# Optimization experiments

Measured on AMD Instinct MI355X. Metric: run time of the kernel, lower is better.

Reference implementation:

```python
import jax, jax.numpy as jnp
import numpy as np

DELTA_VAR = 0.5
DELTA_DIST = 1.5
ALPHA = 1.0
BETA = 1.0
GAMMA = 0.001
NUM_INST = 32  # instance ids are 1..NUM_INST; 0 = background


def setup_inputs() -> dict:
    key = jax.random.key(0)
    k1, k2 = jax.random.split(key)
    embeddings = jax.random.normal(k1, (4, 16, 512, 512), dtype=jnp.float32)
    instance_labels = jax.random.randint(k2, (4, 512, 512), 0, NUM_INST + 1, dtype=jnp.int32)
    return {"embeddings": embeddings, "instance_labels": instance_labels}


def reference(embeddings, instance_labels):
    B, E, H, W = embeddings.shape
    HW = H * W
    S = NUM_INST + 1  # segment slots per batch incl. background slot 0

    emb = embeddings.transpose(0, 2, 3, 1).reshape(B, HW, E)   # [B, HW, E]
    lab = instance_labels.reshape(B, HW)                        # [B, HW]

    # ---- per-(batch, instance) means via one segment reduction ----
    seg = (jnp.arange(B, dtype=lab.dtype)[:, None] * S + lab).reshape(-1)
    sums = jax.ops.segment_sum(emb.reshape(-1, E), seg, num_segments=B * S).reshape(B, S, E)
    counts = jax.ops.segment_sum(jnp.ones((B * HW,), emb.dtype), seg, num_segments=B * S).reshape(B, S)
    means = sums / jnp.maximum(counts, 1.0)[..., None]          # [B, S, E]

    present = counts[:, 1:] > 0                                  # [B, K] instances only
    n = present.sum(-1).astype(emb.dtype)                        # [B] num_instances
    n_safe = jnp.maximum(n, 1.0)

    # ---- variance (pull) term: hinge(||e - mean||_2 - delta_var) ----
    mean_per_pix = jnp.take_along_axis(means, lab[:, :, None], axis=1)  # [B, HW, E]
    diff = emb - mean_per_pix
    pix_dist = jnp.sqrt(jnp.sum(diff * diff, axis=-1))           # [B, HW] (norm=2)
    hinge = jnp.maximum(pix_dist - DELTA_VAR, 0.0) * (lab > 0).astype(emb.dtype)
    var_loss = hinge.sum(-1) / n_safe                            # [B]

    # ---- distance (push) term: pairwise hinge(2*delta_dist - ||mi - mj||) ----
    m = means[:, 1:]                                             # [B, K, E]
    d2 = jnp.sum((m[:, :, None, :] - m[:, None, :, :]) ** 2, -1)  # [B, K, K]
    upper = jnp.triu(jnp.ones((NUM_INST, NUM_INST), bool), 1)
    pair_mask = upper[None] & present[:, :, None] & present[:, None, :]
    d = jnp.sqrt(jnp.where(pair_mask, d2, 1.0))
    pair_hinge = jnp.where(pair_mask, jnp.maximum(2.0 * DELTA_DIST - d, 0.0), 0.0)
    num_pairs = n * (n - 1.0) / 2.0
    dist_loss = jnp.where(n > 1, pair_hinge.sum((-1, -2)) / jnp.maximum(num_pairs, 1.0), 0.0)  # [B]

    # ---- regularization term: ||mean||_2 averaged over instances ----
    mnorm = jnp.sqrt(jnp.where(present, jnp.sum(m * m, -1), 1.0))
    reg_loss = jnp.where(present, mnorm, 0.0).sum(-1) / n_safe   # [B]

    total = ALPHA * var_loss.mean() + BETA * dist_loss.mean() + GAMMA * reg_loss.mean()
    return total
```

## Files before the change

### kernel.cpp

```cpp
#include <hip/hip_runtime.h>

#define NB 4
#define NE 16
#define NHW (512*512)
#define NINST 32
#define SP 17
#define DELTA_VAR 0.5f
#define DELTA_DIST 1.5f
#define ALPHA 1.0f
#define BETA 1.0f
#define GAMMA 0.001f

typedef __attribute__((ext_vector_type(8))) short short8;
typedef __attribute__((ext_vector_type(4))) float f32x4;

#define T_SUM 0
#define T_CNT (NB*NINST*NE)
#define T_MEAN (T_CNT + NB*NINST)
#define T_VARP (T_MEAN + NB*33*NE)
#define T_DIST (T_VARP+NB)
#define T_REG  (T_DIST+NB)
#define T_NS   (T_REG+NB)
#define T_TOTAL (T_NS+NB)

#define GRID_H 1024
#define BLK_H 256
#define BPB_H (GRID_H/NB)
#define PXB 1024
#define PXW 256
#define ITERS_H 4
#define GRID_V 1024
#define BLK_V 256
#define BPB_V (GRID_V/NB)

__device__ __forceinline__ unsigned f2bf(float x) {
    unsigned u = __builtin_bit_cast(unsigned, x);
    return (u + 0x7FFFu + ((u >> 16) & 1u)) >> 16;
}

__device__ __forceinline__ float wave_sum(float v) {
    #pragma unroll
    for (int o = 32; o > 0; o >>= 1) v += __shfl_down(v, o, 64);
    return v;
}

union PK { unsigned u[4]; short8 s; };

__global__ __launch_bounds__(BLK_H) void k_hist(const float* __restrict__ emb,
        const int* __restrict__ lab, float* __restrict__ tbl) {
    __shared__ float red[4][2*NE][SP];
    __shared__ float redc[4][2*NE];
    const int t = threadIdx.x;
    const int lane = t & 63;
    const int wv = t >> 6;
    const int colg = lane >> 4;
    const int cm = lane & 15;
    const int b = blockIdx.x / BPB_H;
    const int blk = blockIdx.x % BPB_H;

    const float* ebase = emb + (size_t)b*(NE*NHW) + (size_t)cm*NHW;
    const int* lbase = lab + (size_t)b*NHW;

    f32x4 acc_s0 = {0.f,0.f,0.f,0.f}, acc_s1 = {0.f,0.f,0.f,0.f};
    f32x4 acc_c0 = {0.f,0.f,0.f,0.f}, acc_c1 = {0.f,0.f,0.f,0.f};
    PK ones; ones.u[0]=ones.u[1]=ones.u[2]=ones.u[3]=0x3F803F80u;

    const int base = blk*PXB + wv*PXW;
    for (int it = 0; it < ITERS_H; ++it) {
        #pragma unroll
        for (int u2 = 0; u2 < 2; ++u2) {
            const int ko = base + it*64 + u2*32 + colg*8;
            const float4 v0 = *(const float4*)(ebase + ko);
            const float4 v1 = *(const float4*)(ebase + ko + 4);
            const int4 L0 = *(const int4*)(lbase + ko);
            const int4 L1 = *(const int4*)(lbase + ko + 4);
            PK bf;
            bf.u[0] = f2bf(v0.x) | (f2bf(v0.y) << 16);
            bf.u[1] = f2bf(v0.z) | (f2bf(v0.w) << 16);
            bf.u[2] = f2bf(v1.x) | (f2bf(v1.y) << 16);
            bf.u[3] = f2bf(v1.z) | (f2bf(v1.w) << 16);
            const int la[8] = {L0.x,L0.y,L0.z,L0.w,L1.x,L1.y,L1.z,L1.w};
            PK a0, a1;
            #pragma unroll
            for (int p = 0; p < 4; ++p) {
                const unsigned lo0 = (la[2*p]   == cm+1 ) ? 0x3F80u : 0u;
                const unsigned hi0 = (la[2*p+1] == cm+1 ) ? 0x3F80u : 0u;
                const unsigned lo1 = (la[2*p]   == cm+17) ? 0x3F80u : 0u;
                const unsigned hi1 = (la[2*p+1] == cm+17) ? 0x3F80u : 0u;
                a0.u[p] = lo0 | (hi0 << 16);
                a1.u[p] = lo1 | (hi1 << 16);
            }
            acc_s0 = __builtin_amdgcn_mfma_f32_16x16x32_bf16(a0.s, bf.s,  acc_s0, 0,0,0);
            acc_s1 = __builtin_amdgcn_mfma_f32_16x16x32_bf16(a1.s, bf.s,  acc_s1, 0,0,0);
            acc_c0 = __builtin_amdgcn_mfma_f32_16x16x32_bf16(a0.s, ones.s, acc_c0, 0,0,0);
            acc_c1 = __builtin_amdgcn_mfma_f32_16x16x32_bf16(a1.s, ones.s, acc_c1, 0,0,0);
        }
    }
    #pragma unroll
    for (int r = 0; r < 4; ++r) {
        red[wv][colg*4 + r][cm]      = acc_s0[r];
        red[wv][16 + colg*4 + r][cm] = acc_s1[r];
    }
    if (cm == 0) {
        #pragma unroll
        for (int r = 0; r < 4; ++r) {
            redc[wv][colg*4 + r]      = acc_c0[r];
            redc[wv][16 + colg*4 + r] = acc_c1[r];
        }
    }
    __syncthreads();
    for (int i = t; i < NINST*NE; i += BLK_H) {
        const int s = i >> 4, e = i & 15;
        const float v = red[0][s][e] + red[1][s][e] + red[2][s][e] + red[3][s][e];
        atomicAdd(&tbl[T_SUM + b*NINST*NE + i], v);
    }
    if (t < NINST) {
        const float v = redc[0][t] + redc[1][t] + redc[2][t] + redc[3][t];
        atomicAdd(&tbl[T_CNT + b*NINST + t], v);
    }
}

__global__ void k_stats(float* __restrict__ tbl) {
    const int b = blockIdx.x;
    const int lane = threadIdx.x;
    __shared__ float lcnt[NINST];
    __shared__ float lmean[NINST*SP];
    __shared__ int lpres[NINST];
    if (lane < NINST) {
        const float c = tbl[T_CNT + b*NINST + lane];
        lcnt[lane] = c;
        lpres[lane] = (c > 0.f) ? 1 : 0;
    }
    __syncthreads();
    for (int i = lane; i < NINST*NE; i += 64) {
        const int s = i >> 4, e = i & 15;
        const float m = tbl[T_SUM + b*NINST*NE + i] / fmaxf(lcnt[s], 1.f);
        lmean[s*SP + e] = m;
        tbl[T_MEAN + b*33*NE + (s+1)*NE + e] = m;
    }
    if (lane < NE) tbl[T_MEAN + b*33*NE + lane] = 0.f;
    __syncthreads();
    const int n = __popcll(__ballot((lane < NINST) ? (lpres[lane] != 0) : false));
    float dsum = 0.f;
    for (int idx = lane; idx < NINST*NINST; idx += 64) {
        const int i = idx >> 5, j = idx & 31;
        if (i < j && lpres[i] && lpres[j]) {
            float d2 = 0.f;
            #pragma unroll
            for (int e = 0; e < NE; e++) {
                const float df = lmean[i*SP+e] - lmean[j*SP+e];
                d2 += df*df;
            }
            dsum += fmaxf(2.f*DELTA_DIST - sqrtf(d2), 0.f);
        }
    }
    dsum = wave_sum(dsum);
    float rsum = 0.f;
    if (lane < NINST && lpres[lane]) {
        float s2 = 0.f;
        #pragma unroll
        for (int e = 0; e < NE; e++) { const float m = lmean[lane*SP+e]; s2 += m*m; }
        rsum = sqrtf(s2);
    }
    rsum = wave_sum(rsum);
    if (lane == 0) {
        const float nf = (float)n;
        const float nsafe = fmaxf(nf, 1.f);
        tbl[T_DIST+b] = (n > 1) ? dsum / fmaxf(nf*(nf-1.f)*0.5f, 1.f) : 0.f;
        tbl[T_REG+b] = rsum / nsafe;
        tbl[T_NS+b] = nsafe;
    }
}

__global__ __launch_bounds__(BLK_V) void k_var(const float* __restrict__ emb,
        const int* __restrict__ lab, float* __restrict__ tbl) {
    __shared__ float lmean[33*SP];
    __shared__ float lvar;
    const int t = threadIdx.x;
    const int b = blockIdx.x / BPB_V;
    const int blk = blockIdx.x % BPB_V;
    for (int i = t; i < 33*NE; i += BLK_V) {
        const int s = i >> 4, e = i & 15;
        lmean[s*SP+e] = tbl[T_MEAN + b*33*NE + i];
        (void)s; (void)e;
    }
    __syncthreads();
    if (t == 0) lvar = 0.f;
    __syncthreads();
    const float* ebase = emb + (size_t)b*(NE*NHW);
    const int* lbase = lab + (size_t)b*NHW;
    float acc = 0.f;
    for (int q = blk*BLK_V + t; q < NHW/4; q += BPB_V*BLK_V) {
        const int p = q*4;
        const int4 l4 = *(const int4*)(lbase + p);
        const int o0 = l4.x*SP, o1 = l4.y*SP, o2 = l4.z*SP, o3 = l4.w*SP;
        float d0=0.f, d1=0.f, d2=0.f, d3=0.f;
        #pragma unroll
        for (int e = 0; e < NE; e++) {
            const float4 v = *(const float4*)(ebase + (size_t)e*NHW + p);
            float df;
            df = v.x - lmean[o0+e]; d0 += df*df;
            df = v.y - lmean[o1+e]; d1 += df*df;
            df = v.z - lmean[o2+e]; d2 += df*df;
            df = v.w - lmean[o3+e]; d3 += df*df;
        }
        if (l4.x > 0) acc += fmaxf(sqrtf(d0) - DELTA_VAR, 0.f);
        if (l4.y > 0) acc += fmaxf(sqrtf(d1) - DELTA_VAR, 0.f);
        if (l4.z > 0) acc += fmaxf(sqrtf(d2) - DELTA_VAR, 0.f);
        if (l4.w > 0) acc += fmaxf(sqrtf(d3) - DELTA_VAR, 0.f);
    }
    const float w = wave_sum(acc);
    if ((t & 63) == 0) atomicAdd(&lvar, w);
    __syncthreads();
    if (t == 0) atomicAdd(&tbl[T_VARP+b], lvar);
}

__global__ void k_final(const float* __restrict__ tbl, float* __restrict__ out) {
    if (threadIdx.x == 0 && blockIdx.x == 0) {
        float tot = 0.f;
        for (int b = 0; b < NB; b++) {
            tot += ALPHA * (tbl[T_VARP+b] / tbl[T_NS+b])
                 + BETA * tbl[T_DIST+b]
                 + GAMMA * tbl[T_REG+b];
        }
        out[0] = tot * (1.f/NB);
    }
}

extern "C" void kernel_launch(void* const* d_in, const int* in_sizes, int n_in,
                              void* d_out, int out_size, void* d_ws, size_t ws_size,
                              hipStream_t stream) {
    const float* emb = (const float*)d_in[0];
    const int* lab = (const int*)d_in[1];
    float* out = (float*)d_out;
    float* tbl = (float*)d_ws;

    hipMemsetAsync(d_ws, 0, (size_t)T_TOTAL*sizeof(float), stream);
    k_hist<<<GRID_H, BLK_H, 0, stream>>>(emb, lab, tbl);
    k_stats<<<NB, 64, 0, stream>>>(tbl);
    k_var<<<GRID_V, BLK_V, 0, stream>>>(emb, lab, tbl);
    k_final<<<1, 64, 0, stream>>>(tbl, out);
}
```

Baseline: 61.90 us.

## Replace global atomics with per-block partials and replicate means in LDS

The histogram kernel now writes per-block partial sums to workspace with 256 blocks of 512 threads, and the stats kernel reduces them. This removes the global atomics and the memset launch. The variance kernel drops its grid-stride loop so each thread handles one group of four pixels. It also loads means from a 4-way replicated, 20-float-padded LDS table as float4 vectors to cut bank conflicts. Per-block variance partials are summed in the final kernel instead of through atomics. The cost is more workspace traffic and a serial partial reduction over 64 blocks in k_stats.

```diff
diff --git a/kernel.cpp b/kernel.cpp
--- a/kernel.cpp
+++ b/kernel.cpp
@@ -4,7 +4,6 @@
 #define NE 16
 #define NHW (512*512)
 #define NINST 32
-#define SP 17
 #define DELTA_VAR 0.5f
 #define DELTA_DIST 1.5f
 #define ALPHA 1.0f
@@ -14,25 +13,28 @@
 typedef __attribute__((ext_vector_type(8))) short short8;
 typedef __attribute__((ext_vector_type(4))) float f32x4;
 
-#define T_SUM 0
-#define T_CNT (NB*NINST*NE)
-#define T_MEAN (T_CNT + NB*NINST)
-#define T_VARP (T_MEAN + NB*33*NE)
-#define T_DIST (T_VARP+NB)
-#define T_REG  (T_DIST+NB)
-#define T_NS   (T_REG+NB)
-#define T_TOTAL (T_NS+NB)
-
-#define GRID_H 1024
-#define BLK_H 256
+#define PH_STRIDE 544
+#define GRID_H 256
+#define P_HIST 0
+#define T_MEAN (GRID_H*PH_STRIDE)
+#define T_MEAN_SZ (33*16)
+#define T_DIST (T_MEAN + NB*T_MEAN_SZ)
+#define T_REG  (T_DIST + NB)
+#define T_NS   (T_REG + NB)
+#define V_PART (T_NS + NB)
+
+#define BLK_H 512
 #define BPB_H (GRID_H/NB)
-#define PXB 1024
-#define PXW 256
-#define ITERS_H 4
+#define PXB_H 4096
+#define PXW_H 512
+#define CHUNKS_H 16
 #define GRID_V 1024
 #define BLK_V 256
 #define BPB_V (GRID_V/NB)
 
+#define LMREP 4
+#define LMSTR 668
+
 __device__ __forceinline__ unsigned f2bf(float x) {
     unsigned u = __builtin_bit_cast(unsigned, x);
     return (u + 0x7FFFu + ((u >> 16) & 1u)) >> 16;
@@ -47,9 +49,9 @@
 union PK { unsigned u[4]; short8 s; };
 
 __global__ __launch_bounds__(BLK_H) void k_hist(const float* __restrict__ emb,
-        const int* __restrict__ lab, float* __restrict__ tbl) {
-    __shared__ float red[4][2*NE][SP];
-    __shared__ float redc[4][2*NE];
+        const int* __restrict__ lab, float* __restrict__ ws) {
+    __shared__ float red[8][2*NE][17];
+    __shared__ float redc[8][2*NE];
     const int t = threadIdx.x;
     const int lane = t & 63;
     const int wv = t >> 6;
@@ -65,36 +67,34 @@
     f32x4 acc_c0 = {0.f,0.f,0.f,0.f}, acc_c1 = {0.f,0.f,0.f,0.f};
     PK ones; ones.u[0]=ones.u[1]=ones.u[2]=ones.u[3]=0x3F803F80u;
 
-    const int base = blk*PXB + wv*PXW;
-    for (int it = 0; it < ITERS_H; ++it) {
+    const int base = blk*PXB_H + wv*PXW_H;
+    #pragma unroll 4
+    for (int it = 0; it < CHUNKS_H; ++it) {
+        const int ko = base + it*32 + colg*8;
+        const float4 v0 = *(const float4*)(ebase + ko);
+        const float4 v1 = *(const float4*)(ebase + ko + 4);
+        const int4 L0 = *(const int4*)(lbase + ko);
+        const int4 L1 = *(const int4*)(lbase + ko + 4);
+        PK bf;
+        bf.u[0] = f2bf(v0.x) | (f2bf(v0.y) << 16);
+        bf.u[1] = f2bf(v0.z) | (f2bf(v0.w) << 16);
+        bf.u[2] = f2bf(v1.x) | (f2bf(v1.y) << 16);
+        bf.u[3] = f2bf(v1.z) | (f2bf(v1.w) << 16);
+        const int la[8] = {L0.x,L0.y,L0.z,L0.w,L1.x,L1.y,L1.z,L1.w};
+        PK a0, a1;
         #pragma unroll
-        for (int u2 = 0; u2 < 2; ++u2) {
-            const int ko = base + it*64 + u2*32 + colg*8;
-            const float4 v0 = *(const float4*)(ebase + ko);
-            const float4 v1 = *(const float4*)(ebase + ko + 4);
-            const int4 L0 = *(const int4*)(lbase + ko);
-            const int4 L1 = *(const int4*)(lbase + ko + 4);
-            PK bf;
-            bf.u[0] = f2bf(v0.x) | (f2bf(v0.y) << 16);
-            bf.u[1] = f2bf(v0.z) | (f2bf(v0.w) << 16);
-            bf.u[2] = f2bf(v1.x) | (f2bf(v1.y) << 16);
-            bf.u[3] = f2bf(v1.z) | (f2bf(v1.w) << 16);
-            const int la[8] = {L0.x,L0.y,L0.z,L0.w,L1.x,L1.y,L1.z,L1.w};
-            PK a0, a1;
-            #pragma unroll
-            for (int p = 0; p < 4; ++p) {
-                const unsigned lo0 = (la[2*p]   == cm+1 ) ? 0x3F80u : 0u;
-                const unsigned hi0 = (la[2*p+1] == cm+1 ) ? 0x3F80u : 0u;
-                const unsigned lo1 = (la[2*p]   == cm+17) ? 0x3F80u : 0u;
-                const unsigned hi1 = (la[2*p+1] == cm+17) ? 0x3F80u : 0u;
-                a0.u[p] = lo0 | (hi0 << 16);
-                a1.u[p] = lo1 | (hi1 << 16);
-            }
-            acc_s0 = __builtin_amdgcn_mfma_f32_16x16x32_bf16(a0.s, bf.s,  acc_s0, 0,0,0);
-            acc_s1 = __builtin_amdgcn_mfma_f32_16x16x32_bf16(a1.s, bf.s,  acc_s1, 0,0,0);
-            acc_c0 = __builtin_amdgcn_mfma_f32_16x16x32_bf16(a0.s, ones.s, acc_c0, 0,0,0);
-            acc_c1 = __builtin_amdgcn_mfma_f32_16x16x32_bf16(a1.s, ones.s, acc_c1, 0,0,0);
-        }
+        for (int p = 0; p < 4; ++p) {
+            const unsigned lo0 = (la[2*p]   == cm+1 ) ? 0x3F80u : 0u;
+            const unsigned hi0 = (la[2*p+1] == cm+1 ) ? 0x3F80u : 0u;
+            const unsigned lo1 = (la[2*p]   == cm+17) ? 0x3F80u : 0u;
+            const unsigned hi1 = (la[2*p+1] == cm+17) ? 0x3F80u : 0u;
+            a0.u[p] = lo0 | (hi0 << 16);
+            a1.u[p] = lo1 | (hi1 << 16);
+        }
+        acc_s0 = __builtin_amdgcn_mfma_f32_16x16x32_bf16(a0.s, bf.s,   acc_s0, 0,0,0);
+        acc_s1 = __builtin_amdgcn_mfma_f32_16x16x32_bf16(a1.s, bf.s,   acc_s1, 0,0,0);
+        acc_c0 = __builtin_amdgcn_mfma_f32_16x16x32_bf16(a0.s, ones.s, acc_c0, 0,0,0);
+        acc_c1 = __builtin_amdgcn_mfma_f32_16x16x32_bf16(a1.s, ones.s, acc_c1, 0,0,0);
     }
     #pragma unroll
     for (int r = 0; r < 4; ++r) {
@@ -109,119 +109,153 @@
         }
     }
     __syncthreads();
-    for (int i = t; i < NINST*NE; i += BLK_H) {
+    float* dst = ws + P_HIST + (size_t)blockIdx.x*PH_STRIDE;
+    for (int i = t; i < PH_STRIDE; i += BLK_H) {
+        float v;
+        if (i < 512) {
+            const int s = i >> 4, e = i & 15;
+            v = red[0][s][e]+red[1][s][e]+red[2][s][e]+red[3][s][e]
+              + red[4][s][e]+red[5][s][e]+red[6][s][e]+red[7][s][e];
+        } else {
+            const int s = i - 512;
+            v = redc[0][s]+redc[1][s]+redc[2][s]+redc[3][s]
+              + redc[4][s]+redc[5][s]+redc[6][s]+redc[7][s];
+        }
+        dst[i] = v;
+    }
+}
+
+__global__ void k_stats(float* __restrict__ ws) {
+    const int b = blockIdx.x;
+    const int t = threadIdx.x;
+    __shared__ float lred[PH_STRIDE];
+    __shared__ float lmean[NINST*17];
+    __shared__ float lcnt[NINST];
+    __shared__ int lpres[NINST];
+    const float* ph = ws + P_HIST + (size_t)(b*BPB_H)*PH_STRIDE;
+    for (int i = t; i < PH_STRIDE; i += 256) {
+        float s = 0.f;
+        #pragma unroll 8
+        for (int k = 0; k < BPB_H; k++) s += ph[(size_t)k*PH_STRIDE + i];
+        lred[i] = s;
+    }
+    __syncthreads();
+    if (t < NINST) {
+        const float c = lred[512 + t];
+        lcnt[t] = c;
+        lpres[t] = (c > 0.f) ? 1 : 0;
+    }
+    __syncthreads();
+    for (int i = t; i < 512; i += 256) {
         const int s = i >> 4, e = i & 15;
-        const float v = red[0][s][e] + red[1][s][e] + red[2][s][e] + red[3][s][e];
-        atomicAdd(&tbl[T_SUM + b*NINST*NE + i], v);
-    }
-    if (t < NINST) {
-        const float v = redc[0][t] + redc[1][t] + redc[2][t] + redc[3][t];
-        atomicAdd(&tbl[T_CNT + b*NINST + t], v);
-    }
-}
-
-__global__ void k_stats(float* __restrict__ tbl) {
-    const int b = blockIdx.x;
-    const int lane = threadIdx.x;
-    __shared__ float lcnt[NINST];
-    __shared__ float lmean[NINST*SP];
-    __shared__ int lpres[NINST];
-    if (lane < NINST) {
-        const float c = tbl[T_CNT + b*NINST + lane];
-        lcnt[lane] = c;
-        lpres[lane] = (c > 0.f) ? 1 : 0;
-    }
-    __syncthreads();
-    for (int i = lane; i < NINST*NE; i += 64) {
-        const int s = i >> 4, e = i & 15;
-        const float m = tbl[T_SUM + b*NINST*NE + i] / fmaxf(lcnt[s], 1.f);
-        lmean[s*SP + e] = m;
-        tbl[T_MEAN + b*33*NE + (s+1)*NE + e] = m;
-    }
-    if (lane < NE) tbl[T_MEAN + b*33*NE + lane] = 0.f;
-    __syncthreads();
-    const int n = __popcll(__ballot((lane < NINST) ? (lpres[lane] != 0) : false));
-    float dsum = 0.f;
-    for (int idx = lane; idx < NINST*NINST; idx += 64) {
-        const int i = idx >> 5, j = idx & 31;
-        if (i < j && lpres[i] && lpres[j]) {
-            float d2 = 0.f;
+        lmean[s*17 + e] = lred[i] / fmaxf(lcnt[s], 1.f);
+    }
+    __syncthreads();
+    for (int i = t; i < 33*NE; i += 256) {
+        const int l = i >> 4, e = i & 15;
+        ws[T_MEAN + b*T_MEAN_SZ + i] = (l == 0) ? 0.f : lmean[(l-1)*17 + e];
+    }
+    if (t < 64) {
+        const int lane = t;
+        const int n = __popcll(__ballot((lane < NINST) ? (lpres[lane] != 0) : false));
+        float dsum = 0.f;
+        for (int idx = lane; idx < NINST*NINST; idx += 64) {
+            const int i = idx >> 5, j = idx & 31;
+            if (i < j && lpres[i] && lpres[j]) {
+                float d2 = 0.f;
+                #pragma unroll
+                for (int e = 0; e < NE; e++) {
+                    const float df = lmean[i*17+e] - lmean[j*17+e];
+                    d2 += df*df;
+                }
+                dsum += fmaxf(2.f*DELTA_DIST - sqrtf(d2), 0.f);
+            }
+        }
+        dsum = wave_sum(dsum);
+        float rsum = 0.f;
+        if (lane < NINST && lpres[lane]) {
+            float s2 = 0.f;
             #pragma unroll
-            for (int e = 0; e < NE; e++) {
-                const float df = lmean[i*SP+e] - lmean[j*SP+e];
-                d2 += df*df;
-            }
-            dsum += fmaxf(2.f*DELTA_DIST - sqrtf(d2), 0.f);
-        }
-    }
-    dsum = wave_sum(dsum);
-    float rsum = 0.f;
-    if (lane < NINST && lpres[lane]) {
-        float s2 = 0.f;
-        #pragma unroll
-        for (int e = 0; e < NE; e++) { const float m = lmean[lane*SP+e]; s2 += m*m; }
-        rsum = sqrtf(s2);
-    }
-    rsum = wave_sum(rsum);
-    if (lane == 0) {
-        const float nf = (float)n;
-        const float nsafe = fmaxf(nf, 1.f);
-        tbl[T_DIST+b] = (n > 1) ? dsum / fmaxf(nf*(nf-1.f)*0.5f, 1.f) : 0.f;
-        tbl[T_REG+b] = rsum / nsafe;
-        tbl[T_NS+b] = nsafe;
+            for (int e = 0; e < NE; e++) { const float m = lmean[lane*17+e]; s2 += m*m; }
+            rsum = sqrtf(s2);
+        }
+        rsum = wave_sum(rsum);
+        if (lane == 0) {
+            const float nf = (float)n;
+            const float nsafe = fmaxf(nf, 1.f);
+            ws[T_DIST+b] = (n > 1) ? dsum / fmaxf(nf*(nf-1.f)*0.5f, 1.f) : 0.f;
+            ws[T_REG+b] = rsum / nsafe;
+            ws[T_NS+b] = nsafe;
+        }
     }
 }
 
 __global__ __launch_bounds__(BLK_V) void k_var(const float* __restrict__ emb,
-        const int* __restrict__ lab, float* __restrict__ tbl) {
-    __shared__ float lmean[33*SP];
-    __shared__ float lvar;
-    const int t = threadIdx.x;
-    const int b = blockIdx.x / BPB_V;
-    const int blk = blockIdx.x % BPB_V;
-    for (int i = t; i < 33*NE; i += BLK_V) {
-        const int s = i >> 4, e = i & 15;
-        lmean[s*SP+e] = tbl[T_MEAN + b*33*NE + i];
-        (void)s; (void)e;
-    }
-    __syncthreads();
-    if (t == 0) lvar = 0.f;
-    __syncthreads();
+        const int* __restrict__ lab, float* __restrict__ ws) {
+    __shared__ __align__(16) float lm[LMREP*LMSTR];
+    __shared__ float wred[4];
+    const int t = threadIdx.x;
+    const int b = blockIdx.x >> 8;
+    const int blk = blockIdx.x & 255;
+    for (int c4 = 0; c4 < LMREP; ++c4) {
+        for (int i = t; i < 33*20; i += BLK_V) {
+            const int l = i / 20, e = i % 20;
+            if (e < 16) lm[c4*LMSTR + i] = ws[T_MEAN + b*T_MEAN_SZ + l*16 + e];
+        }
+    }
+    __syncthreads();
+    const float* lmc = lm + ((t >> 4) & (LMREP-1))*LMSTR;
     const float* ebase = emb + (size_t)b*(NE*NHW);
     const int* lbase = lab + (size_t)b*NHW;
+
+    const int p = (blk*BLK_V + t)*4;
+    const int4 l4 = *(const int4*)(lbase + p);
+    float4 m0[4], m1[4], m2[4], m3[4];
+    {
+        const float4* q0 = (const float4*)(lmc + l4.x*20);
+        const float4* q1 = (const float4*)(lmc + l4.y*20);
+        const float4* q2 = (const float4*)(lmc + l4.z*20);
+        const float4* q3 = (const float4*)(lmc + l4.w*20);
+        #pragma unroll
+        for (int c = 0; c < 4; ++c) { m0[c]=q0[c]; m1[c]=q1[c]; m2[c]=q2[c]; m3[c]=q3[c]; }
+    }
+    float d0=0.f, d1=0.f, d2=0.f, d3=0.f;
+    #pragma unroll
+    for (int e = 0; e < NE; e++) {
+        const float4 v = *(const float4*)(ebase + (size_t)e*NHW + p);
+        float df;
+        df = v.x - ((const float*)&m0[e>>2])[e&3]; d0 += df*df;
+        df = v.y - ((const float*)&m1[e>>2])[e&3]; d1 += df*df;
+        df = v.z - ((const float*)&m2[e>>2])[e&3]; d2 += df*df;
+        df = v.w - ((const float*)&m3[e>>2])[e&3]; d3 += df*df;
+    }
     float acc = 0.f;
-    for (int q = blk*BLK_V + t; q < NHW/4; q += BPB_V*BLK_V) {
-        const int p = q*4;
-        const int4 l4 = *(const int4*)(lbase + p);
-        const int o0 = l4.x*SP, o1 = l4.y*SP, o2 = l4.z*SP, o3 = l4.w*SP;
-        float d0=0.f, d1=0.f, d2=0.f, d3=0.f;
-        #pragma unroll
-        for (int e = 0; e < NE; e++) {
-            const float4 v = *(const float4*)(ebase + (size_t)e*NHW + p);
-            float df;
-            df = v.x - lmean[o0+e]; d0 += df*df;
-            df = v.y - lmean[o1+e]; d1 += df*df;
-            df = v.z - lmean[o2+e]; d2 += df*df;
-            df = v.w - lmean[o3+e]; d3 += df*df;
-        }
-        if (l4.x > 0) acc += fmaxf(sqrtf(d0) - DELTA_VAR, 0.f);
-        if (l4.y > 0) acc += fmaxf(sqrtf(d1) - DELTA_VAR, 0.f);
-        if (l4.z > 0) acc += fmaxf(sqrtf(d2) - DELTA_VAR, 0.f);
-        if (l4.w > 0) acc += fmaxf(sqrtf(d3) - DELTA_VAR, 0.f);
-    }
-    const float w = wave_sum(acc);
-    if ((t & 63) == 0) atomicAdd(&lvar, w);
-    __syncthreads();
-    if (t == 0) atomicAdd(&tbl[T_VARP+b], lvar);
-}
-
-__global__ void k_final(const float* __restrict__ tbl, float* __restrict__ out) {
-    if (threadIdx.x == 0 && blockIdx.x == 0) {
+    if (l4.x > 0) acc += fmaxf(sqrtf(d0) - DELTA_VAR, 0.f);
+    if (l4.y > 0) acc += fmaxf(sqrtf(d1) - DELTA_VAR, 0.f);
+    if (l4.z > 0) acc += fmaxf(sqrtf(d2) - DELTA_VAR, 0.f);
+    if (l4.w > 0) acc += fmaxf(sqrtf(d3) - DELTA_VAR, 0.f);
+
+    const float wsum = wave_sum(acc);
+    if ((t & 63) == 0) wred[t >> 6] = wsum;
+    __syncthreads();
+    if (t == 0) ws[V_PART + blockIdx.x] = wred[0]+wred[1]+wred[2]+wred[3];
+}
+
+__global__ void k_final(const float* __restrict__ ws, float* __restrict__ out) {
+    const int t = threadIdx.x;
+    __shared__ float vb[4];
+    float s = 0.f;
+    #pragma unroll
+    for (int k = 0; k < 4; ++k) s += ws[V_PART + t*4 + k];
+    s = wave_sum(s);
+    if ((t & 63) == 0) vb[t >> 6] = s;
+    __syncthreads();
+    if (t == 0) {
         float tot = 0.f;
         for (int b = 0; b < NB; b++) {
-            tot += ALPHA * (tbl[T_VARP+b] / tbl[T_NS+b])
-                 + BETA * tbl[T_DIST+b]
-                 + GAMMA * tbl[T_REG+b];
+            tot += ALPHA * (vb[b] / ws[T_NS+b])
+                 + BETA * ws[T_DIST+b]
+                 + GAMMA * ws[T_REG+b];
         }
         out[0] = tot * (1.f/NB);
     }
@@ -233,11 +267,10 @@
     const float* emb = (const float*)d_in[0];
     const int* lab = (const int*)d_in[1];
     float* out = (float*)d_out;
-    float* tbl = (float*)d_ws;
-
-    hipMemsetAsync(d_ws, 0, (size_t)T_TOTAL*sizeof(float), stream);
-    k_hist<<<GRID_H, BLK_H, 0, stream>>>(emb, lab, tbl);
-    k_stats<<<NB, 64, 0, stream>>>(tbl);
-    k_var<<<GRID_V, BLK_V, 0, stream>>>(emb, lab, tbl);
-    k_final<<<1, 64, 0, stream>>>(tbl, out);
-}
+    float* ws = (float*)d_ws;
+
+    k_hist<<<GRID_H, BLK_H, 0, stream>>>(emb, lab, ws);
+    k_stats<<<NB, 256, 0, stream>>>(ws);
+    k_var<<<GRID_V, BLK_V, 0, stream>>>(emb, lab, ws);
+    k_final<<<1, 256, 0, stream>>>(ws, out);
+}
```

Result: faster. 53.46 us (-13.6%).
